# Optimization experiments

Hardware: AMD Instinct MI355X
Metric: run time of the kernel (lower is better)

## Reference

```python
import jax, jax.numpy as jnp
import numpy as np

B, C, N, T = 16, 32, 1024, 64
C_OUT = 32
ORDER = 2
SMOOTH_DEPTH = 1


def setup_inputs() -> dict:
    key = jax.random.key(0)
    k1, k2, k3, k4 = jax.random.split(key, 4)
    x = jax.random.normal(k1, (B, C, N, T), dtype=jnp.float32)
    # row-normalized dense adjacencies (transition matrices), as used in Graph-WaveNet-style supports
    AL = jax.random.uniform(k2, (N, N), dtype=jnp.float32)
    AL = AL / AL.sum(axis=-1, keepdims=True)
    AS_pos = jax.random.uniform(k3, (N, N), dtype=jnp.float32)
    AS_pos = AS_pos / AS_pos.sum(axis=-1, keepdims=True)
    # 1x1 conv mlp: in_channels = (order*support_len+1)*c_in = 3*C, out_channels = C_OUT
    W_mlp = jax.random.normal(k4, (C_OUT, (ORDER + 1) * C), dtype=jnp.float32) * 0.02
    b_mlp = jnp.zeros((C_OUT,), dtype=jnp.float32)
    return {"x": x, "AL": AL, "AS_pos": AS_pos, "W_mlp": W_mlp, "b_mlp": b_mlp}


def reference(x, AL, AS_pos, W_mlp, b_mlp):
    # gcn_module.forward with short_bool=True, smooth_depth=SMOOTH_DEPTH, eval mode (no dropout)
    ALp = jnp.linalg.matrix_power(AL, SMOOTH_DEPTH)          # [N,N]
    # torch.einsum('bckj,ik->bcij', x, ALp): contract node dim of x against ALp
    x_long = jnp.einsum('ik,bckt->bcit', ALp, x)             # [B,C,N,T]
    x_short = x - x_long
    outs = [x]
    for _ in range(ORDER):
        # dnconv: einsum('nvw,ncwl->ncvl', A, x) with 2D A broadcast over batch
        x_long = jnp.einsum('vw,bcwt->bcvt', AL, x_long)
        x_short = jnp.einsum('vw,bcwt->bcvt', AS_pos, x_short)
        outs.append(x_long + x_short)
    h = jnp.concatenate(outs, axis=1)                        # [B,(ORDER+1)*C,N,T]
    # 1x1 conv == channel mixing
    h = jnp.einsum('oc,bcnt->bont', W_mlp, h) + b_mlp[None, :, None, None]
    return h
```

## Files before the change

### kernel.cpp

```cpp
#include <hip/hip_runtime.h>


typedef __bf16 bf16x8 __attribute__((ext_vector_type(8)));
typedef float f32x4 __attribute__((ext_vector_type(4)));
typedef unsigned int u32x4 __attribute__((ext_vector_type(4)));
typedef unsigned int u32x2 __attribute__((ext_vector_type(2)));

__device__ __forceinline__ unsigned short f2bf(float f) {
  unsigned u = __builtin_bit_cast(unsigned, f);
  u += 0x7fffu + ((u >> 16) & 1u);
  return (unsigned short)(u >> 16);
}
__device__ __forceinline__ float bf2f(unsigned short h) {
  unsigned u = ((unsigned)h) << 16;
  return __builtin_bit_cast(float, u);
}

static constexpr size_t OFF_XT    = 0;
static constexpr size_t OFF_U     = 67108864;
static constexpr size_t OFF_ALBF  = 201326592;
static constexpr size_t OFF_ALT   = OFF_ALBF  + 2097152;
static constexpr size_t OFF_ASBF  = OFF_ALT   + 2097152;
static constexpr size_t OFF_AST   = OFF_ASBF  + 2097152;
static constexpr size_t OFF_AL2   = OFF_AST   + 2097152;
static constexpr size_t OFF_AL2T  = OFF_AL2   + 2097152;
static constexpr size_t OFF_ASAL  = OFF_AL2T  + 2097152;
static constexpr size_t OFF_AS2   = OFF_ASAL  + 2097152;
static constexpr size_t OFF_AL3   = OFF_AS2   + 2097152;
static constexpr size_t OFF_AS2AL = OFF_AL3   + 2097152;
static constexpr size_t OFF_G     = OFF_AS2AL + 2097152;

__global__ __launch_bounds__(256) void k_cast_bf16(const float* __restrict__ src,
                                                   unsigned short* __restrict__ dst,
                                                   int n4) {
  int i = blockIdx.x * 256 + threadIdx.x;
  if (i < n4) {
    float4 v = *((const float4*)src + i);
    unsigned lo = (unsigned)f2bf(v.x) | ((unsigned)f2bf(v.y) << 16);
    unsigned hi = (unsigned)f2bf(v.z) | ((unsigned)f2bf(v.w) << 16);
    u32x2 pk = {lo, hi};
    *(u32x2*)(dst + (size_t)i * 4) = pk;
  }
}

__global__ __launch_bounds__(256) void k_transpose_cast(const float* __restrict__ src,
                                                        unsigned short* __restrict__ dst,
                                                        int R, int Cc) {
  __shared__ float Xs[64][65];
  const int tid = threadIdx.x;
  const size_t slice = (size_t)blockIdx.z * (size_t)R * (size_t)Cc;
  const float* s = src + slice;
  unsigned short* d = dst + slice;
  const int r0 = blockIdx.x * 64, c0 = blockIdx.y * 64;
  const int lrow = tid >> 4, lc4 = tid & 15;
#pragma unroll
  for (int rr = 0; rr < 4; rr++) {
    int row = rr * 16 + lrow;
    float4 v = *(const float4*)(s + (size_t)(r0 + row) * Cc + c0 + lc4 * 4);
    Xs[row][lc4 * 4 + 0] = v.x;
    Xs[row][lc4 * 4 + 1] = v.y;
    Xs[row][lc4 * 4 + 2] = v.z;
    Xs[row][lc4 * 4 + 3] = v.w;
  }
  __syncthreads();
  const int wc = tid & 7;
#pragma unroll
  for (int u = 0; u < 2; u++) {
    int t = u * 32 + (tid >> 3);
    unsigned v0 = (unsigned)f2bf(Xs[wc * 8 + 0][t]) | ((unsigned)f2bf(Xs[wc * 8 + 1][t]) << 16);
    unsigned v1 = (unsigned)f2bf(Xs[wc * 8 + 2][t]) | ((unsigned)f2bf(Xs[wc * 8 + 3][t]) << 16);
    unsigned v2 = (unsigned)f2bf(Xs[wc * 8 + 4][t]) | ((unsigned)f2bf(Xs[wc * 8 + 5][t]) << 16);
    unsigned v3 = (unsigned)f2bf(Xs[wc * 8 + 6][t]) | ((unsigned)f2bf(Xs[wc * 8 + 7][t]) << 16);
    u32x4 pk = {v0, v1, v2, v3};
    *(u32x4*)(d + (size_t)(c0 + t) * R + r0 + wc * 8) = pk;
  }
}

__device__ __forceinline__ void gemm128_bt(const unsigned short* __restrict__ A,
                                           const unsigned short* __restrict__ Bt,
                                           unsigned short* __restrict__ Cp,
                                           int K, size_t ldc, int m0, int n0) {
  __shared__ unsigned short As[128 * 32];
  __shared__ unsigned short Bs[128 * 32];
  const int tid = threadIdx.x;
  const int wave = tid >> 6, lane = tid & 63;
  const int lane15 = lane & 15, quad = lane >> 4;
  const int wm = wave & 1, wn = wave >> 1;
  const int srow = lane >> 2;
  const int schunk = (lane & 3) * 8;

  const unsigned short* gA0 = A + (size_t)(m0 + wave * 16 + srow) * K + schunk;
  const unsigned short* gA1 = A + (size_t)(m0 + 64 + wave * 16 + srow) * K + schunk;
  const unsigned short* gB0 = Bt + (size_t)(n0 + wave * 16 + srow) * K + schunk;
  const unsigned short* gB1 = Bt + (size_t)(n0 + 64 + wave * 16 + srow) * K + schunk;
  unsigned short* lA0 = As + (wave * 16) * 32;
  unsigned short* lA1 = As + (64 + wave * 16) * 32;
  unsigned short* lB0 = Bs + (wave * 16) * 32;
  unsigned short* lB1 = Bs + (64 + wave * 16) * 32;

  f32x4 acc[4][4];
#pragma unroll
  for (int i = 0; i < 4; i++)
#pragma unroll
    for (int j = 0; j < 4; j++) acc[i][j] = (f32x4){0.f, 0.f, 0.f, 0.f};

  const unsigned short* pa = As + (wm * 64 + lane15) * 32 + quad * 8;
  const unsigned short* pb = Bs + (wn * 64 + lane15) * 32 + quad * 8;

  for (int kb = 0; kb < K; kb += 32) {
    __syncthreads();
    __builtin_amdgcn_global_load_lds(
        (const __attribute__((address_space(1))) unsigned int*)(gA0 + kb),
        (__attribute__((address_space(3))) unsigned int*)lA0, 16, 0, 0);
    __builtin_amdgcn_global_load_lds(
        (const __attribute__((address_space(1))) unsigned int*)(gA1 + kb),
        (__attribute__((address_space(3))) unsigned int*)lA1, 16, 0, 0);
    __builtin_amdgcn_global_load_lds(
        (const __attribute__((address_space(1))) unsigned int*)(gB0 + kb),
        (__attribute__((address_space(3))) unsigned int*)lB0, 16, 0, 0);
    __builtin_amdgcn_global_load_lds(
        (const __attribute__((address_space(1))) unsigned int*)(gB1 + kb),
        (__attribute__((address_space(3))) unsigned int*)lB1, 16, 0, 0);
    __syncthreads();

    bf16x8 av[4], bv[4];
#pragma unroll
    for (int mt = 0; mt < 4; mt++) av[mt] = *(const bf16x8*)(pa + mt * 16 * 32);
#pragma unroll
    for (int nt = 0; nt < 4; nt++) bv[nt] = *(const bf16x8*)(pb + nt * 16 * 32);
#pragma unroll
    for (int mt = 0; mt < 4; mt++)
#pragma unroll
      for (int nt = 0; nt < 4; nt++)
        acc[mt][nt] = __builtin_amdgcn_mfma_f32_16x16x32_bf16(av[mt], bv[nt], acc[mt][nt], 0, 0, 0);
  }

#pragma unroll
  for (int mt = 0; mt < 4; mt++) {
#pragma unroll
    for (int nt = 0; nt < 4; nt++) {
      const int col = n0 + wn * 64 + nt * 16 + lane15;
#pragma unroll
      for (int r = 0; r < 4; r++) {
        const int row = m0 + wm * 64 + mt * 16 + quad * 4 + r;
        Cp[(size_t)row * ldc + col] = f2bf(acc[mt][nt][r]);
      }
    }
  }
}

__global__ __launch_bounds__(256) void k_gemm_pre(char* ws, int stage) {
  const unsigned short* A;
  const unsigned short* Bt;
  unsigned short* Cp;
  const int z = blockIdx.z;
  unsigned short* ALbf = (unsigned short*)(ws + OFF_ALBF);
  unsigned short* ALt  = (unsigned short*)(ws + OFF_ALT);
  unsigned short* ASbf = (unsigned short*)(ws + OFF_ASBF);
  unsigned short* ASt  = (unsigned short*)(ws + OFF_AST);
  unsigned short* AL2  = (unsigned short*)(ws + OFF_AL2);
  unsigned short* AL2t = (unsigned short*)(ws + OFF_AL2T);
  unsigned short* ASAL = (unsigned short*)(ws + OFF_ASAL);
  unsigned short* AS2  = (unsigned short*)(ws + OFF_AS2);
  unsigned short* AL3  = (unsigned short*)(ws + OFF_AL3);
  unsigned short* AS2AL= (unsigned short*)(ws + OFF_AS2AL);
  if (stage == 0) {
    if (z == 0)      { A = ALbf; Bt = ALt;  Cp = AL2;  }
    else if (z == 1) { A = ALt;  Bt = ALbf; Cp = AL2t; }
    else if (z == 2) { A = ASbf; Bt = ALt;  Cp = ASAL; }
    else             { A = ASbf; Bt = ASt;  Cp = AS2;  }
  } else {
    if (z == 0)      { A = ALbf; Bt = AL2t; Cp = AL3;  }
    else             { A = AS2;  Bt = ALt;  Cp = AS2AL;}
  }
  gemm128_bt(A, Bt, Cp, 1024, 1024, blockIdx.y * 128, blockIdx.x * 128);
}

__global__ __launch_bounds__(256) void k_assemble_G(const unsigned short* __restrict__ AL2,
                                                    const unsigned short* __restrict__ ASAL,
                                                    const float* __restrict__ ASf,
                                                    const unsigned short* __restrict__ AL3,
                                                    const unsigned short* __restrict__ AS2,
                                                    const unsigned short* __restrict__ AS2AL,
                                                    unsigned short* __restrict__ G) {
  int i = blockIdx.x * 256 + threadIdx.x;
  float g1 = bf2f(AL2[i]) + ASf[i] - bf2f(ASAL[i]);
  G[i] = f2bf(g1);
  float g2 = bf2f(AL3[i]) + bf2f(AS2[i]) - bf2f(AS2AL[i]);
  G[1048576 + i] = f2bf(g2);
}

__global__ __launch_bounds__(512) void k_gemm_main8(const unsigned short* __restrict__ A,
                                                    const unsigned short* __restrict__ Bt,
                                                    unsigned short* __restrict__ C) {
  __shared__ unsigned short lds[65536];
  const int tid = threadIdx.x;
  const int wave = tid >> 6, lane = tid & 63;
  const int lane15 = lane & 15, quad = lane >> 4;
  const int wr = wave >> 2, wc = wave & 3;

  const int bid = blockIdx.x;
  const int swz = (bid & 7) * 128 + (bid >> 3);
  const int nx = swz >> 3, my = swz & 7;
  const int m0 = my * 256, n0 = nx * 256;

  const int srow = tid >> 3;
  const int skc  = (((tid & 7) ^ (srow & 7)) << 3);
  const int ldst0 = (tid & ~63) << 3;

#define STAGE_HALF(gbase, rowbase, ldsptr, ktile)                                       \
  do {                                                                                  \
    const unsigned short* _g =                                                          \
        (gbase) + (size_t)((rowbase) + srow) * 1024 + (size_t)((ktile) * 64 + skc);     \
    __builtin_amdgcn_global_load_lds(                                                   \
        (const __attribute__((address_space(1))) unsigned int*)_g,                      \
        (__attribute__((address_space(3))) unsigned int*)((ldsptr) + ldst0), 16, 0, 0); \
    __builtin_amdgcn_global_load_lds(                                                   \
        (const __attribute__((address_space(1))) unsigned int*)(_g + 65536),            \
        (__attribute__((address_space(3))) unsigned int*)((ldsptr) + 4096 + ldst0),     \
        16, 0, 0);                                                                      \
  } while (0)

#define LOAD_AFR(p)                                                                     \
  bf16x8 afr[2][2];                                                                     \
  _Pragma("unroll") for (int mi = 0; mi < 2; mi++)                                      \
      _Pragma("unroll") for (int kk = 0; kk < 2; kk++)                                  \
          afr[mi][kk] = *(const bf16x8*)(pA + (2 * (p) + mi) * 1024 + aks[kk]);

#define MFMA_QUAD(p)                                                                    \
  _Pragma("unroll") for (int kk = 0; kk < 2; kk++)                                      \
      _Pragma("unroll") for (int mi = 0; mi < 2; mi++)                                  \
          _Pragma("unroll") for (int n = 0; n < 4; n++)                                 \
              acc[2 * (p) + mi][n] = __builtin_amdgcn_mfma_f32_16x16x32_bf16(           \
                  afr[mi][kk], bfr[n][kk], acc[2 * (p) + mi][n], 0, 0, 0);

#define PHASE_SYNC_PRE()                              \
  asm volatile("" ::: "memory");                      \
  __builtin_amdgcn_s_barrier();                       \
  asm volatile("s_waitcnt lgkmcnt(0)" ::: "memory");  \
  __builtin_amdgcn_sched_barrier(0);                  \
  __builtin_amdgcn_s_setprio(1);

#define PHASE_SYNC_POST()                             \
  __builtin_amdgcn_s_setprio(0);                      \
  asm volatile("" ::: "memory");                      \
  __builtin_amdgcn_s_barrier();

  unsigned short* Acur = lds;
  unsigned short* Bcur = lds + 16384;
  unsigned short* Aalt = lds + 32768;
  unsigned short* Balt = lds + 49152;

  f32x4 acc[8][4];
#pragma unroll
  for (int i = 0; i < 8; i++)
#pragma unroll
    for (int j = 0; j < 4; j++) acc[i][j] = (f32x4){0.f, 0.f, 0.f, 0.f};

  const int swz8 = (lane15 & 7) << 3;
  int aks[2];
  aks[0] = (quad << 3) ^ swz8;
  aks[1] = (32 | (quad << 3)) ^ swz8;

  STAGE_HALF(Bt, n0,       Bcur,        0);
  STAGE_HALF(Bt, n0 + 128, Bcur + 8192, 0);
  STAGE_HALF(A,  m0,       Acur,        0);
  STAGE_HALF(A,  m0 + 128, Acur + 8192, 0);
  STAGE_HALF(Bt, n0,       Balt,        1);
  STAGE_HALF(Bt, n0 + 128, Balt + 8192, 1);
  STAGE_HALF(A,  m0,       Aalt,        1);
  asm volatile("s_waitcnt vmcnt(6)" ::: "memory");
  __builtin_amdgcn_s_barrier();

  for (int u = 0; u < 14; ++u) {
    const unsigned short* pA = Acur + (wr * 128 + lane15) * 64;
    const unsigned short* pB = Bcur + (wc * 64 + lane15) * 64;
    bf16x8 bfr[4][2];
    {
#pragma unroll
      for (int n = 0; n < 4; n++)
#pragma unroll
        for (int kk = 0; kk < 2; kk++)
          bfr[n][kk] = *(const bf16x8*)(pB + n * 1024 + aks[kk]);
      LOAD_AFR(0)
      __builtin_amdgcn_sched_barrier(0);
      STAGE_HALF(A, m0 + 128, Aalt + 8192, u + 1);
      asm volatile("s_waitcnt lgkmcnt(8)" ::: "memory");
      PHASE_SYNC_PRE()
      MFMA_QUAD(0)
      PHASE_SYNC_POST()
    }
    {
      LOAD_AFR(1)
      __builtin_amdgcn_sched_barrier(0);
      STAGE_HALF(Bt, n0, Bcur, u + 2);
      PHASE_SYNC_PRE()
      MFMA_QUAD(1)
      PHASE_SYNC_POST()
    }
    {
      LOAD_AFR(2)
      __builtin_amdgcn_sched_barrier(0);
      STAGE_HALF(Bt, n0 + 128, Bcur + 8192, u + 2);
      PHASE_SYNC_PRE()
      MFMA_QUAD(2)
      PHASE_SYNC_POST()
    }
    {
      LOAD_AFR(3)
      __builtin_amdgcn_sched_barrier(0);
      STAGE_HALF(A, m0, Acur, u + 2);
      PHASE_SYNC_PRE()
      MFMA_QUAD(3)
      __builtin_amdgcn_s_setprio(0);
      asm volatile("s_waitcnt vmcnt(6)" ::: "memory");
      asm volatile("" ::: "memory");
      __builtin_amdgcn_s_barrier();
    }
    unsigned short* t;
    t = Acur; Acur = Aalt; Aalt = t;
    t = Bcur; Bcur = Balt; Balt = t;
  }

  {
    const unsigned short* pA = Acur + (wr * 128 + lane15) * 64;
    const unsigned short* pB = Bcur + (wc * 64 + lane15) * 64;
    bf16x8 bfr[4][2];
    {
#pragma unroll
      for (int n = 0; n < 4; n++)
#pragma unroll
        for (int kk = 0; kk < 2; kk++)
          bfr[n][kk] = *(const bf16x8*)(pB + n * 1024 + aks[kk]);
      LOAD_AFR(0)
      __builtin_amdgcn_sched_barrier(0);
      STAGE_HALF(A, m0 + 128, Aalt + 8192, 15);
      asm volatile("s_waitcnt lgkmcnt(8)" ::: "memory");
      PHASE_SYNC_PRE()
      MFMA_QUAD(0)
      PHASE_SYNC_POST()
    }
    { LOAD_AFR(1) PHASE_SYNC_PRE() MFMA_QUAD(1) PHASE_SYNC_POST() }
    { LOAD_AFR(2) PHASE_SYNC_PRE() MFMA_QUAD(2) PHASE_SYNC_POST() }
    {
      LOAD_AFR(3)
      PHASE_SYNC_PRE()
      MFMA_QUAD(3)
      __builtin_amdgcn_s_setprio(0);
      asm volatile("s_waitcnt vmcnt(0)" ::: "memory");
      asm volatile("" ::: "memory");
      __builtin_amdgcn_s_barrier();
    }
    unsigned short* t;
    t = Acur; Acur = Aalt; Aalt = t;
    t = Bcur; Bcur = Balt; Balt = t;
  }

  {
    const unsigned short* pA = Acur + (wr * 128 + lane15) * 64;
    const unsigned short* pB = Bcur + (wc * 64 + lane15) * 64;
    bf16x8 bfr[4][2];
#pragma unroll
    for (int n = 0; n < 4; n++)
#pragma unroll
      for (int kk = 0; kk < 2; kk++)
        bfr[n][kk] = *(const bf16x8*)(pB + n * 1024 + aks[kk]);
#pragma unroll
    for (int p = 0; p < 4; p++) {
      bf16x8 afr[2][2];
#pragma unroll
      for (int mi = 0; mi < 2; mi++)
#pragma unroll
        for (int kk = 0; kk < 2; kk++)
          afr[mi][kk] = *(const bf16x8*)(pA + (2 * p + mi) * 1024 + aks[kk]);
#pragma unroll
      for (int kk = 0; kk < 2; kk++)
#pragma unroll
        for (int mi = 0; mi < 2; mi++)
#pragma unroll
          for (int n = 0; n < 4; n++)
            acc[2 * p + mi][n] = __builtin_amdgcn_mfma_f32_16x16x32_bf16(
                afr[mi][kk], bfr[n][kk], acc[2 * p + mi][n], 0, 0, 0);
    }
  }

#pragma unroll
  for (int mt = 0; mt < 8; mt++) {
    const int row = m0 + wr * 128 + mt * 16 + quad * 4;
#pragma unroll
    for (int n = 0; n < 4; n++) {
      const int col = n0 + wc * 64 + n * 16 + lane15;
#pragma unroll
      for (int r = 0; r < 4; r++)
        C[(size_t)(row + r) * 32768 + col] = f2bf(acc[mt][n][r]);
    }
  }
#undef STAGE_HALF
#undef LOAD_AFR
#undef MFMA_QUAD
#undef PHASE_SYNC_PRE
#undef PHASE_SYNC_POST
}

__device__ __forceinline__ int swz_off(int j, int kc) {
  int s = (j ^ (j >> 3) ^ (j >> 6)) & 7;
  return (kc ^ s) << 3;
}

__global__ __launch_bounds__(256) void k_mix_mfma(const float* __restrict__ x,
                                                  const unsigned short* __restrict__ U,
                                                  const unsigned short* __restrict__ Wbf,
                                                  const float* __restrict__ bm,
                                                  float* __restrict__ out) {
  __shared__ unsigned short Hs[128 * 128];
  const int tid = threadIdx.x;
  const int b  = blockIdx.x >> 9;
  const int n0 = (blockIdx.x & 511) * 2;

  const float* xb = x + (size_t)b * 2097152 + (size_t)n0 * 64;
#pragma unroll
  for (int i = 0; i < 4; i++) {
    int q = tid + 256 * i;
    int p = q >> 4;
    int c = p >> 1, nn = p & 1;
    int t0 = (q & 15) * 4;
    float4 v = *(const float4*)(xb + (size_t)c * 65536 + nn * 64 + t0);
    int kc = c >> 3, wi = c & 7;
    float vv[4] = {v.x, v.y, v.z, v.w};
#pragma unroll
    for (int e = 0; e < 4; e++) {
      int j = nn * 64 + t0 + e;
      Hs[j * 128 + swz_off(j, kc) + wi] = f2bf(vv[e]);
    }
  }
#pragma unroll
  for (int i = 0; i < 4; i++) {
    int q = tid + 256 * i;
    int row = q >> 8;
    int g = row >> 1, nn = row & 1;
    int s8 = (q & 255) * 8;
    int c = s8 >> 6;
    const unsigned short* src =
        U + (size_t)(g * 1024 + n0 + nn) * 32768 + (size_t)b * 2048 + s8;
    u32x4 v = *(const u32x4*)src;
    int kc = 4 + g * 4 + (c >> 3), wi = c & 7;
#pragma unroll
    for (int e = 0; e < 4; e++) {
      int j0 = nn * 64 + (s8 & 63) + 2 * e;
      unsigned w = v[e];
      Hs[j0 * 128 + swz_off(j0, kc) + wi]           = (unsigned short)(w & 0xffffu);
      Hs[(j0 + 1) * 128 + swz_off(j0 + 1, kc) + wi] = (unsigned short)(w >> 16);
    }
  }
  __syncthreads();

  const int wave = tid >> 6, lane = tid & 63;
  const int lane15 = lane & 15, quad = lane >> 4;
  f32x4 acc[2][2];
#pragma unroll
  for (int jt = 0; jt < 2; jt++)
#pragma unroll
    for (int ot = 0; ot < 2; ot++) acc[jt][ot] = (f32x4){0.f, 0.f, 0.f, 0.f};

#pragma unroll
  for (int kchunk = 0; kchunk < 3; kchunk++) {
    bf16x8 bv[2];
#pragma unroll
    for (int ot = 0; ot < 2; ot++)
      bv[ot] = *(const bf16x8*)(Wbf + (ot * 16 + lane15) * 96 + kchunk * 32 + quad * 8);
#pragma unroll
    for (int jt = 0; jt < 2; jt++) {
      int j = wave * 32 + jt * 16 + lane15;
      bf16x8 av = *(const bf16x8*)(Hs + j * 128 + swz_off(j, kchunk * 4 + quad));
#pragma unroll
      for (int ot = 0; ot < 2; ot++)
        acc[jt][ot] = __builtin_amdgcn_mfma_f32_16x16x32_bf16(av, bv[ot], acc[jt][ot], 0, 0, 0);
    }
  }

#pragma unroll
  for (int jt = 0; jt < 2; jt++) {
#pragma unroll
    for (int ot = 0; ot < 2; ot++) {
      int col = ot * 16 + lane15;
      float bo = bm[col];
#pragma unroll
      for (int r = 0; r < 4; r++) {
        int j = wave * 32 + jt * 16 + quad * 4 + r;
        int nn = j >> 6, t = j & 63;
        out[(size_t)b * 2097152 + (size_t)col * 65536 + (size_t)(n0 + nn) * 64 + t] =
            acc[jt][ot][r] + bo;
      }
    }
  }
}

extern "C" void kernel_launch(void* const* d_in, const int* in_sizes, int n_in,
                              void* d_out, int out_size, void* d_ws, size_t ws_size,
                              hipStream_t stream) {
  const float* x  = (const float*)d_in[0];
  const float* AL = (const float*)d_in[1];
  const float* AS = (const float*)d_in[2];
  const float* W  = (const float*)d_in[3];
  const float* bm = (const float*)d_in[4];
  float* out = (float*)d_out;
  char* ws = (char*)d_ws;

  unsigned short* xT    = (unsigned short*)(ws + OFF_XT);
  unsigned short* U     = (unsigned short*)(ws + OFF_U);
  unsigned short* ALbf  = (unsigned short*)(ws + OFF_ALBF);
  unsigned short* ALt   = (unsigned short*)(ws + OFF_ALT);
  unsigned short* ASbf  = (unsigned short*)(ws + OFF_ASBF);
  unsigned short* ASt   = (unsigned short*)(ws + OFF_AST);
  unsigned short* AL2   = (unsigned short*)(ws + OFF_AL2);
  unsigned short* ASAL  = (unsigned short*)(ws + OFF_ASAL);
  unsigned short* AS2   = (unsigned short*)(ws + OFF_AS2);
  unsigned short* AL3   = (unsigned short*)(ws + OFF_AL3);
  unsigned short* AS2AL = (unsigned short*)(ws + OFF_AS2AL);
  unsigned short* Gm    = (unsigned short*)(ws + OFF_G);
  unsigned short* Wbf   = (unsigned short*)(ws + OFF_ALBF);

  k_cast_bf16<<<1024, 256, 0, stream>>>(AL, ALbf, 262144);
  k_cast_bf16<<<1024, 256, 0, stream>>>(AS, ASbf, 262144);
  k_transpose_cast<<<dim3(16, 16, 1), 256, 0, stream>>>(AL, ALt, 1024, 1024);
  k_transpose_cast<<<dim3(16, 16, 1), 256, 0, stream>>>(AS, ASt, 1024, 1024);
  k_transpose_cast<<<dim3(16, 1, 512), 256, 0, stream>>>(x, xT, 1024, 64);
  k_gemm_pre<<<dim3(8, 8, 4), 256, 0, stream>>>(ws, 0);
  k_gemm_pre<<<dim3(8, 8, 2), 256, 0, stream>>>(ws, 1);
  k_assemble_G<<<4096, 256, 0, stream>>>(AL2, ASAL, AS, AL3, AS2, AS2AL, Gm);
  k_cast_bf16<<<3, 256, 0, stream>>>(W, Wbf, 768);
  k_gemm_main8<<<dim3(1024, 1, 1), 512, 0, stream>>>(Gm, xT, U);
  k_mix_mfma<<<dim3(8192, 1, 1), 256, 0, stream>>>(x, U, Wbf, bm, out);
}
```

Measured before the change: 497.4 us.

## Apply channel-mixing weights before graph GEMM and fuse output epilogue

Reorders the computation so the 1x1 channel-mix weights are applied to x first (k_mix_g), producing per-output-channel projections that are then contracted against the concatenated [G1|G2] graph operator in a single K=2048 GEMM. The GEMM epilogue adds the W0·x term and bias and writes fp32 output directly. This removes the separate x transpose, the large intermediate U buffer, and the mixing kernel's reload of U. The cost is a longer K loop, a 32-wide output instead of 64 rows of GEMM work, and strided scalar x loads plus scattered bf16 stores in k_mix_g.

```diff
diff --git a/kernel.cpp b/kernel.cpp
--- a/kernel.cpp
+++ b/kernel.cpp
@@ -16,8 +16,8 @@
   return __builtin_bit_cast(float, u);
 }
 
-static constexpr size_t OFF_XT    = 0;
-static constexpr size_t OFF_U     = 67108864;
+static constexpr size_t OFF_YC    = 0;
+static constexpr size_t OFF_Y0    = 134217728;
 static constexpr size_t OFF_ALBF  = 201326592;
 static constexpr size_t OFF_ALT   = OFF_ALBF  + 2097152;
 static constexpr size_t OFF_ASBF  = OFF_ALT   + 2097152;
@@ -40,6 +40,16 @@
     unsigned hi = (unsigned)f2bf(v.z) | ((unsigned)f2bf(v.w) << 16);
     u32x2 pk = {lo, hi};
     *(u32x2*)(dst + (size_t)i * 4) = pk;
+  }
+}
+
+__global__ __launch_bounds__(256) void k_cast_wall(const float* __restrict__ W,
+                                                   unsigned short* __restrict__ Wall) {
+  int i = blockIdx.x * 256 + threadIdx.x;
+  if (i < 3072) {
+    int oo = i >> 5, c = i & 31;
+    int o = oo & 31, g = oo >> 5;
+    Wall[i] = f2bf(W[o * 96 + g * 32 + c]);
   }
 }
 
@@ -184,15 +194,86 @@
                                                     const unsigned short* __restrict__ AS2AL,
                                                     unsigned short* __restrict__ G) {
   int i = blockIdx.x * 256 + threadIdx.x;
+  int r = i >> 10, c = i & 1023;
   float g1 = bf2f(AL2[i]) + ASf[i] - bf2f(ASAL[i]);
-  G[i] = f2bf(g1);
   float g2 = bf2f(AL3[i]) + bf2f(AS2[i]) - bf2f(AS2AL[i]);
-  G[1048576 + i] = f2bf(g2);
+  G[(size_t)r * 2048 + c]        = f2bf(g1);
+  G[(size_t)r * 2048 + 1024 + c] = f2bf(g2);
+}
+
+__global__ __launch_bounds__(256) void k_mix_g(const float* __restrict__ x,
+                                               const unsigned short* __restrict__ Wall,
+                                               unsigned short* __restrict__ Yc,
+                                               unsigned short* __restrict__ Y0v) {
+  const int tid = threadIdx.x;
+  const int b  = blockIdx.x >> 4;
+  const int n0 = (blockIdx.x & 15) * 64;
+  const int wave = tid >> 6, lane = tid & 63;
+  const int lane15 = lane & 15, quad = lane >> 4;
+  const int t = wave * 16 + lane15;
+
+  bf16x8 afr[6];
+#pragma unroll
+  for (int ot = 0; ot < 6; ot++)
+    afr[ot] = *(const bf16x8*)(Wall + (ot * 16 + lane15) * 32 + quad * 8);
+
+  const float* xb = x + (size_t)b * 2097152 + (size_t)(quad * 8) * 65536 + t;
+
+  for (int ng = 0; ng < 8; ng++) {
+    const int nbase = n0 + ng * 8;
+    bf16x8 bfr[8];
+#pragma unroll
+    for (int nl = 0; nl < 8; nl++) {
+      const float* xp = xb + (size_t)(nbase + nl) * 64;
+      unsigned u[4];
+#pragma unroll
+      for (int e = 0; e < 4; e++) {
+        float a  = xp[(size_t)(2 * e) * 65536];
+        float c2 = xp[(size_t)(2 * e + 1) * 65536];
+        u[e] = (unsigned)f2bf(a) | ((unsigned)f2bf(c2) << 16);
+      }
+      u32x4 pk = {u[0], u[1], u[2], u[3]};
+      bfr[nl] = __builtin_bit_cast(bf16x8, pk);
+    }
+
+#pragma unroll
+    for (int ot = 0; ot < 6; ot++) {
+      f32x4 acc[8];
+      const f32x4 z = (f32x4){0.f, 0.f, 0.f, 0.f};
+#pragma unroll
+      for (int nl = 0; nl < 8; nl++)
+        acc[nl] = __builtin_amdgcn_mfma_f32_16x16x32_bf16(afr[ot], bfr[nl], z, 0, 0, 0);
+      const int og = ot >> 1;
+      const int o  = (ot & 1) * 16 + quad * 4;
+      if (og == 0) {
+#pragma unroll
+        for (int r = 0; r < 4; r++) {
+          size_t jb = (size_t)(b * 32 + o + r) * 64 + t;
+#pragma unroll
+          for (int nl = 0; nl < 8; nl++)
+            Y0v[(size_t)(nbase + nl) * 32768 + jb] = f2bf(acc[nl][r]);
+        }
+      } else {
+#pragma unroll
+        for (int r = 0; r < 4; r++) {
+          unsigned u0 = (unsigned)f2bf(acc[0][r]) | ((unsigned)f2bf(acc[1][r]) << 16);
+          unsigned u1 = (unsigned)f2bf(acc[2][r]) | ((unsigned)f2bf(acc[3][r]) << 16);
+          unsigned u2 = (unsigned)f2bf(acc[4][r]) | ((unsigned)f2bf(acc[5][r]) << 16);
+          unsigned u3 = (unsigned)f2bf(acc[6][r]) | ((unsigned)f2bf(acc[7][r]) << 16);
+          u32x4 pk = {u0, u1, u2, u3};
+          size_t row = (size_t)(b * 32 + o + r) * 64 + t;
+          *(u32x4*)(Yc + row * 2048 + (og - 1) * 1024 + nbase) = pk;
+        }
+      }
+    }
+  }
 }
 
 __global__ __launch_bounds__(512) void k_gemm_main8(const unsigned short* __restrict__ A,
                                                     const unsigned short* __restrict__ Bt,
-                                                    unsigned short* __restrict__ C) {
+                                                    const unsigned short* __restrict__ Y0v,
+                                                    const float* __restrict__ bm,
+                                                    float* __restrict__ out) {
   __shared__ unsigned short lds[65536];
   const int tid = threadIdx.x;
   const int wave = tid >> 6, lane = tid & 63;
@@ -200,8 +281,8 @@
   const int wr = wave >> 2, wc = wave & 3;
 
   const int bid = blockIdx.x;
-  const int swz = (bid & 7) * 128 + (bid >> 3);
-  const int nx = swz >> 3, my = swz & 7;
+  const int swz = (bid & 7) * 64 + (bid >> 3);
+  const int nx = swz >> 2, my = swz & 3;
   const int m0 = my * 256, n0 = nx * 256;
 
   const int srow = tid >> 3;
@@ -211,12 +292,12 @@
 #define STAGE_HALF(gbase, rowbase, ldsptr, ktile)                                       \
   do {                                                                                  \
     const unsigned short* _g =                                                          \
-        (gbase) + (size_t)((rowbase) + srow) * 1024 + (size_t)((ktile) * 64 + skc);     \
+        (gbase) + (size_t)((rowbase) + srow) * 2048 + (size_t)((ktile) * 64 + skc);     \
     __builtin_amdgcn_global_load_lds(                                                   \
         (const __attribute__((address_space(1))) unsigned int*)_g,                      \
         (__attribute__((address_space(3))) unsigned int*)((ldsptr) + ldst0), 16, 0, 0); \
     __builtin_amdgcn_global_load_lds(                                                   \
-        (const __attribute__((address_space(1))) unsigned int*)(_g + 65536),            \
+        (const __attribute__((address_space(1))) unsigned int*)(_g + 131072),           \
         (__attribute__((address_space(3))) unsigned int*)((ldsptr) + 4096 + ldst0),     \
         16, 0, 0);                                                                      \
   } while (0)
@@ -272,7 +353,7 @@
   asm volatile("s_waitcnt vmcnt(6)" ::: "memory");
   __builtin_amdgcn_s_barrier();
 
-  for (int u = 0; u < 14; ++u) {
+  for (int u = 0; u < 30; ++u) {
     const unsigned short* pA = Acur + (wr * 128 + lane15) * 64;
     const unsigned short* pB = Bcur + (wc * 64 + lane15) * 64;
     bf16x8 bfr[4][2];
@@ -334,7 +415,7 @@
           bfr[n][kk] = *(const bf16x8*)(pB + n * 1024 + aks[kk]);
       LOAD_AFR(0)
       __builtin_amdgcn_sched_barrier(0);
-      STAGE_HALF(A, m0 + 128, Aalt + 8192, 15);
+      STAGE_HALF(A, m0 + 128, Aalt + 8192, 31);
       asm volatile("s_waitcnt lgkmcnt(8)" ::: "memory");
       PHASE_SYNC_PRE()
       MFMA_QUAD(0)
@@ -388,11 +469,16 @@
   for (int mt = 0; mt < 8; mt++) {
     const int row = m0 + wr * 128 + mt * 16 + quad * 4;
 #pragma unroll
-    for (int n = 0; n < 4; n++) {
-      const int col = n0 + wc * 64 + n * 16 + lane15;
-#pragma unroll
-      for (int r = 0; r < 4; r++)
-        C[(size_t)(row + r) * 32768 + col] = f2bf(acc[mt][n][r]);
+    for (int nf = 0; nf < 4; nf++) {
+      const int col = n0 + wc * 64 + nf * 16 + lane15;
+      const int bo_idx = col >> 6;
+      const float bo = bm[bo_idx & 31];
+      const size_t obase = (size_t)bo_idx * 65536 + (col & 63);
+#pragma unroll
+      for (int r = 0; r < 4; r++) {
+        float y0 = bf2f(Y0v[(size_t)(row + r) * 32768 + col]);
+        out[obase + (size_t)(row + r) * 64] = acc[mt][nf][r] + y0 + bo;
+      }
     }
   }
 #undef STAGE_HALF
@@ -400,99 +486,6 @@
 #undef MFMA_QUAD
 #undef PHASE_SYNC_PRE
 #undef PHASE_SYNC_POST
-}
-
-__device__ __forceinline__ int swz_off(int j, int kc) {
-  int s = (j ^ (j >> 3) ^ (j >> 6)) & 7;
-  return (kc ^ s) << 3;
-}
-
-__global__ __launch_bounds__(256) void k_mix_mfma(const float* __restrict__ x,
-                                                  const unsigned short* __restrict__ U,
-                                                  const unsigned short* __restrict__ Wbf,
-                                                  const float* __restrict__ bm,
-                                                  float* __restrict__ out) {
-  __shared__ unsigned short Hs[128 * 128];
-  const int tid = threadIdx.x;
-  const int b  = blockIdx.x >> 9;
-  const int n0 = (blockIdx.x & 511) * 2;
-
-  const float* xb = x + (size_t)b * 2097152 + (size_t)n0 * 64;
-#pragma unroll
-  for (int i = 0; i < 4; i++) {
-    int q = tid + 256 * i;
-    int p = q >> 4;
-    int c = p >> 1, nn = p & 1;
-    int t0 = (q & 15) * 4;
-    float4 v = *(const float4*)(xb + (size_t)c * 65536 + nn * 64 + t0);
-    int kc = c >> 3, wi = c & 7;
-    float vv[4] = {v.x, v.y, v.z, v.w};
-#pragma unroll
-    for (int e = 0; e < 4; e++) {
-      int j = nn * 64 + t0 + e;
-      Hs[j * 128 + swz_off(j, kc) + wi] = f2bf(vv[e]);
-    }
-  }
-#pragma unroll
-  for (int i = 0; i < 4; i++) {
-    int q = tid + 256 * i;
-    int row = q >> 8;
-    int g = row >> 1, nn = row & 1;
-    int s8 = (q & 255) * 8;
-    int c = s8 >> 6;
-    const unsigned short* src =
-        U + (size_t)(g * 1024 + n0 + nn) * 32768 + (size_t)b * 2048 + s8;
-    u32x4 v = *(const u32x4*)src;
-    int kc = 4 + g * 4 + (c >> 3), wi = c & 7;
-#pragma unroll
-    for (int e = 0; e < 4; e++) {
-      int j0 = nn * 64 + (s8 & 63) + 2 * e;
-      unsigned w = v[e];
-      Hs[j0 * 128 + swz_off(j0, kc) + wi]           = (unsigned short)(w & 0xffffu);
-      Hs[(j0 + 1) * 128 + swz_off(j0 + 1, kc) + wi] = (unsigned short)(w >> 16);
-    }
-  }
-  __syncthreads();
-
-  const int wave = tid >> 6, lane = tid & 63;
-  const int lane15 = lane & 15, quad = lane >> 4;
-  f32x4 acc[2][2];
-#pragma unroll
-  for (int jt = 0; jt < 2; jt++)
-#pragma unroll
-    for (int ot = 0; ot < 2; ot++) acc[jt][ot] = (f32x4){0.f, 0.f, 0.f, 0.f};
-
-#pragma unroll
-  for (int kchunk = 0; kchunk < 3; kchunk++) {
-    bf16x8 bv[2];
-#pragma unroll
-    for (int ot = 0; ot < 2; ot++)
-      bv[ot] = *(const bf16x8*)(Wbf + (ot * 16 + lane15) * 96 + kchunk * 32 + quad * 8);
-#pragma unroll
-    for (int jt = 0; jt < 2; jt++) {
-      int j = wave * 32 + jt * 16 + lane15;
-      bf16x8 av = *(const bf16x8*)(Hs + j * 128 + swz_off(j, kchunk * 4 + quad));
-#pragma unroll
-      for (int ot = 0; ot < 2; ot++)
-        acc[jt][ot] = __builtin_amdgcn_mfma_f32_16x16x32_bf16(av, bv[ot], acc[jt][ot], 0, 0, 0);
-    }
-  }
-
-#pragma unroll
-  for (int jt = 0; jt < 2; jt++) {
-#pragma unroll
-    for (int ot = 0; ot < 2; ot++) {
-      int col = ot * 16 + lane15;
-      float bo = bm[col];
-#pragma unroll
-      for (int r = 0; r < 4; r++) {
-        int j = wave * 32 + jt * 16 + quad * 4 + r;
-        int nn = j >> 6, t = j & 63;
-        out[(size_t)b * 2097152 + (size_t)col * 65536 + (size_t)(n0 + nn) * 64 + t] =
-            acc[jt][ot][r] + bo;
-      }
-    }
-  }
 }
 
 extern "C" void kernel_launch(void* const* d_in, const int* in_sizes, int n_in,
@@ -506,8 +499,8 @@
   float* out = (float*)d_out;
   char* ws = (char*)d_ws;
 
-  unsigned short* xT    = (unsigned short*)(ws + OFF_XT);
-  unsigned short* U     = (unsigned short*)(ws + OFF_U);
+  unsigned short* Yc    = (unsigned short*)(ws + OFF_YC);
+  unsigned short* Y0v   = (unsigned short*)(ws + OFF_Y0);
   unsigned short* ALbf  = (unsigned short*)(ws + OFF_ALBF);
   unsigned short* ALt   = (unsigned short*)(ws + OFF_ALT);
   unsigned short* ASbf  = (unsigned short*)(ws + OFF_ASBF);
@@ -518,17 +511,16 @@
   unsigned short* AL3   = (unsigned short*)(ws + OFF_AL3);
   unsigned short* AS2AL = (unsigned short*)(ws + OFF_AS2AL);
   unsigned short* Gm    = (unsigned short*)(ws + OFF_G);
-  unsigned short* Wbf   = (unsigned short*)(ws + OFF_ALBF);
+  unsigned short* Wall  = (unsigned short*)(ws + OFF_ALBF);
 
   k_cast_bf16<<<1024, 256, 0, stream>>>(AL, ALbf, 262144);
   k_cast_bf16<<<1024, 256, 0, stream>>>(AS, ASbf, 262144);
   k_transpose_cast<<<dim3(16, 16, 1), 256, 0, stream>>>(AL, ALt, 1024, 1024);
   k_transpose_cast<<<dim3(16, 16, 1), 256, 0, stream>>>(AS, ASt, 1024, 1024);
-  k_transpose_cast<<<dim3(16, 1, 512), 256, 0, stream>>>(x, xT, 1024, 64);
   k_gemm_pre<<<dim3(8, 8, 4), 256, 0, stream>>>(ws, 0);
   k_gemm_pre<<<dim3(8, 8, 2), 256, 0, stream>>>(ws, 1);
   k_assemble_G<<<4096, 256, 0, stream>>>(AL2, ASAL, AS, AL3, AS2, AS2AL, Gm);
-  k_cast_bf16<<<3, 256, 0, stream>>>(W, Wbf, 768);
-  k_gemm_main8<<<dim3(1024, 1, 1), 512, 0, stream>>>(Gm, xT, U);
-  k_mix_mfma<<<dim3(8192, 1, 1), 256, 0, stream>>>(x, U, Wbf, bm, out);
-}
+  k_cast_wall<<<12, 256, 0, stream>>>(W, Wall);
+  k_mix_g<<<256, 256, 0, stream>>>(x, Wall, Yc, Y0v);
+  k_gemm_main8<<<dim3(512, 1, 1), 512, 0, stream>>>(Gm, Yc, Y0v, bm, out);
+}
```

After: 793.0 us. 59.4% more time.
